# Kernel optimization log

Measured on AMD Instinct MI355X. Metric: run time of the kernel, lower is better.

The kernel has to match this reference:

```python
import jax, jax.numpy as jnp
import numpy as np


def setup_inputs() -> dict:
    key = jax.random.key(0)
    N0, N1, N2, E0, E1 = 40000, 8000, 2000, 128000, 32000
    IN, HID = 512, 256
    ks = iter(jax.random.split(key, 40))
    def nk():
        return next(ks)
    def lin_w(shape):
        fan_in = shape[1]
        return jax.random.uniform(nk(), shape, jnp.float32, -1.0, 1.0) / np.sqrt(fan_in)
    inp = {}
    inp["x"] = jax.random.normal(nk(), (N0, IN), jnp.float32)
    inp["ppr"] = jax.random.uniform(nk(), (N1, N1), jnp.float32) / N1  # ~row-stochastic PPR
    inp["src0"] = jax.random.randint(nk(), (E0,), 0, N0)
    inp["dst0"] = jax.random.randint(nk(), (E0,), 0, N1)
    inp["src1"] = jax.random.randint(nk(), (E1,), 0, N1)
    inp["dst1"] = jax.random.randint(nk(), (E1,), 0, N2)
    inp["n1"] = N1
    inp["n2"] = N2
    # SAGEConv layer 0 (in->hid) and layer 1 (hid->hid); lin_l has bias, lin_r does not (PyG default)
    inp["Wl0"] = lin_w((HID, IN)); inp["bl0"] = jnp.zeros((HID,), jnp.float32); inp["Wr0"] = lin_w((HID, IN))
    inp["Wl1"] = lin_w((HID, HID)); inp["bl1"] = jnp.zeros((HID,), jnp.float32); inp["Wr1"] = lin_w((HID, HID))
    # self.linear = [Linear(IN,IN)+ReLU, Linear(IN,HID)]
    inp["Wa"] = lin_w((IN, IN)); inp["ba"] = jnp.zeros((IN,), jnp.float32)
    inp["Wb"] = lin_w((HID, IN)); inp["bb"] = jnp.zeros((HID,), jnp.float32)
    # lin1 / lin2 (no bias)
    inp["W1"] = lin_w((HID, HID)); inp["W2"] = lin_w((HID, HID))
    # proj = MLP(HID, HID, HID)
    inp["Wp1"] = lin_w((HID, HID)); inp["bp1"] = jnp.zeros((HID,), jnp.float32)
    inp["Wp2"] = lin_w((HID, HID)); inp["bp2"] = jnp.zeros((HID,), jnp.float32)
    # clf = MLP(HID, 32, 1)
    inp["Wc1"] = lin_w((32, HID)); inp["bc1"] = jnp.zeros((32,), jnp.float32)
    inp["Wc2"] = lin_w((1, 32)); inp["bc2"] = jnp.zeros((1,), jnp.float32)
    return inp


def reference(x, ppr, Wl0, bl0, Wr0, Wl1, bl1, Wr1, Wa, ba, Wb, bb,
              W1, W2, Wp1, bp1, Wp2, bp2, Wc1, bc1, Wc2, bc2,
              src0, dst0, src1, dst1, n1, n2):
    EPS = 1e-12
    def l2n(v):
        return v / jnp.maximum(jnp.linalg.norm(v, axis=-1, keepdims=True), EPS)
    def sage(h_src, h_tgt, src, dst, Wl, bl, Wr, n_tgt):
        msg = h_src[src]  # [E, d] gather
        s = jax.ops.segment_sum(msg, dst, num_segments=n_tgt)
        cnt = jax.ops.segment_sum(jnp.ones((dst.shape[0],), h_src.dtype), dst, num_segments=n_tgt)
        agg = s / jnp.maximum(cnt, 1.0)[:, None]  # scatter-mean
        return agg @ Wl.T + bl + h_tgt @ Wr.T
    # --- GraphSAGE encoder (eval mode: dropout no-op) ---
    h = x
    h = sage(h, h[:n1], src0, dst0, Wl0, bl0, Wr0, n1)
    h = jax.nn.relu(h)
    h = sage(h, h[:n2], src1, dst1, Wl1, bl1, Wr1, n2)
    ebds = jax.nn.log_softmax(h, axis=-1)  # output_type 'ebds' != 'ebd' -> log_softmax path
    # --- divergence loss ---
    o1 = l2n(ebds @ W1.T)
    o2 = l2n(ebds @ W2.T)
    div_loss = jnp.mean(jnp.sum((o1 - o2) ** 2, axis=-1))
    # --- PPR branch ---
    xp = ppr[:n1, :n1] @ x[:n1]              # [n1, IN]
    xp = jax.nn.relu(xp @ Wa.T + ba)         # linear[0]
    xp = ppr[:n2, :n2] @ xp[:n2]             # [n2, IN]
    xp = xp @ Wb.T + bb                      # linear[1] -> [n2, HID]
    g1 = l2n(ebds)
    g2 = l2n(xp)
    def proj(v):
        return jax.nn.relu(v @ Wp1.T + bp1) @ Wp2.T + bp2
    def clf(v):
        return jax.nn.relu(v @ Wc1.T + bc1) @ Wc2.T + bc2
    l1 = clf(proj(g1))  # [n2, 1]
    l2_ = clf(proj(g2))  # [n2, 1]
    logits_pair = jnp.concatenate([l1, l2_], axis=-1)  # [n2, 2]
    return logits_pair, div_loss
```

## Files before the change

### kernel.cpp

```cpp
#include <hip/hip_runtime.h>


typedef unsigned short ushort;
typedef __attribute__((ext_vector_type(8))) short short8;
typedef __attribute__((ext_vector_type(4))) float float4v;
typedef __attribute__((ext_vector_type(4))) float f32x4;
typedef __attribute__((ext_vector_type(2))) float f32x2;
typedef __attribute__((ext_vector_type(8))) unsigned short us8;
typedef __attribute__((ext_vector_type(4))) unsigned short us4;
typedef __attribute__((ext_vector_type(2))) unsigned short us2;

__device__ __forceinline__ ushort bf16_rne(float v) {
    unsigned u = __float_as_uint(v);
    u += 0x7fffu + ((u >> 16) & 1u);
    return (ushort)(u >> 16);
}
__device__ __forceinline__ float bf16_f32(ushort h) {
    return __uint_as_float((unsigned)h << 16);
}

constexpr long ZCNT0 = 0;
constexpr long ZCNT1 = 8000;
constexpr long ELL0  = 10240;
constexpr long ELL1  = 522240;
constexpr long H1F   = 650240;
constexpr long H2F   = 2714624;
constexpr long DIVCF = 3238912;
constexpr long XPBF  = 4287488;
constexpr long PB2   = 4811776;
constexpr long PART  = 5860352;
constexpr long FEND  = 10054656;
constexpr long U_PPRB  = 0;
constexpr long U_PPR2B = 16777216;
constexpr long U_XTB   = 20971520;
constexpr long U_XPATB = 25165824;
constexpr long U_A0    = 26214400;
constexpr long U_A1    = 38600704;
constexpr long U_ESPL  = 40697856;
constexpr long U_XPS   = 41746432;
constexpr long U_SPLT  = 43843584;
constexpr long U_TSPL  = 45940736;
constexpr long U_WC0   = 48037888;
constexpr long U_WC1   = 48431104;
constexpr long U_BD    = 48693248;
constexpr long U_WAD   = 48955392;
constexpr long U_WBD   = 49479680;
constexpr long U_WP1D  = 49741824;
constexpr long U_WP2D  = 49872896;
constexpr long U_XB    = 50003968;

__global__ __launch_bounds__(256) void mfma128(
    const ushort* __restrict__ A, const ushort* __restrict__ B,
    float* __restrict__ Cf, ushort* __restrict__ Cs, ushort* __restrict__ Ct,
    const float* __restrict__ bias, int K, int lda, int ldb, int ldc,
    int ldso, int nsplit, int msplit, int ldt, int kchunk, int flags)
{
    __shared__ ushort As[128 * 128];
    __shared__ ushort Bs[128 * 128];
    const int tid = threadIdx.x;
    const int lane = tid & 63, wave = tid >> 6;
    const int wm = (wave >> 1) * 64, wn = (wave & 1) * 64;
    const int lr = lane & 15, quad = lane >> 4;

    int bx = blockIdx.x, by = blockIdx.y;
    if (flags & 8) {
        int gx = gridDim.x;
        int nb = gx * gridDim.y;
        int flat = by * gx + bx;
        int per = nb >> 3;
        int c = flat & 7, j = flat >> 3;
        int idx = c * per + j;
        by = idx / gx; bx = idx % gx;
    }
    const int bm = by * 128, bn = bx * 128;
    const int kbeg = blockIdx.z * kchunk;
    int kend = kbeg + kchunk; if (kend > K) kend = K;

    float4v acc[4][4] = {{{0.f, 0.f, 0.f, 0.f}}};

    for (int k0 = kbeg; k0 < kend; k0 += 128) {
#pragma unroll
        for (int issue = 0; issue < 8; ++issue) {
            int c = issue * 256 + tid;
            int r = c >> 4, p = c & 15;
            int kk = (p ^ (r & 15)) * 8;
            const ushort* ga = A + (long)(bm + r) * lda + k0 + kk;
            const ushort* gb = B + (long)(bn + r) * ldb + k0 + kk;
            __builtin_amdgcn_global_load_lds(
                (const __attribute__((address_space(1))) unsigned int*)ga,
                (__attribute__((address_space(3))) unsigned int*)&As[c * 8], 16, 0, 0);
            __builtin_amdgcn_global_load_lds(
                (const __attribute__((address_space(1))) unsigned int*)gb,
                (__attribute__((address_space(3))) unsigned int*)&Bs[c * 8], 16, 0, 0);
        }
        __syncthreads();

#pragma unroll
        for (int s = 0; s < 4; ++s) {
            short8 af[4], bf[4];
#pragma unroll
            for (int i = 0; i < 4; ++i) {
                int ra = wm + i * 16 + lr;
                af[i] = *(const short8*)&As[ra * 128 + (((s * 4 + quad) ^ (ra & 15)) * 8)];
                int rb = wn + i * 16 + lr;
                bf[i] = *(const short8*)&Bs[rb * 128 + (((s * 4 + quad) ^ (rb & 15)) * 8)];
            }
#pragma unroll
            for (int i = 0; i < 4; ++i)
#pragma unroll
                for (int j = 0; j < 4; ++j)
                    acc[i][j] = __builtin_amdgcn_mfma_f32_16x16x32_bf16(
                        af[i], bf[j], acc[i][j], 0, 0, 0);
        }
        __syncthreads();
    }

    if (gridDim.z > 1) {
        float* Cz = Cf + (long)blockIdx.z * (long)(gridDim.x * 128) * (long)(gridDim.y * 128);
#pragma unroll
        for (int i = 0; i < 4; ++i) {
            int row0 = bm + wm + i * 16 + quad * 4;
#pragma unroll
            for (int j = 0; j < 4; ++j) {
                int col = bn + wn + j * 16 + lr;
#pragma unroll
                for (int r = 0; r < 4; ++r)
                    Cz[(long)(row0 + r) * ldc + col] = acc[i][j][r];
            }
        }
        return;
    }

#pragma unroll
    for (int i = 0; i < 4; ++i) {
        int row0 = bm + wm + i * 16 + quad * 4;
#pragma unroll
        for (int j = 0; j < 4; ++j) {
            int col = bn + wn + j * 16 + lr;
            float bv = bias ? bias[col] : 0.f;
            us4 tp;
#pragma unroll
            for (int r = 0; r < 4; ++r) {
                int row = row0 + r;
                float v = acc[i][j][r] + bv;
                if (flags & 1) v = fmaxf(v, 0.f);
                if (Cf) Cf[(long)row * ldc + col] = v;
                if (Cs && row < msplit) {
                    if (flags & 2) {
                        ushort h = bf16_rne(v);
                        Cs[(long)row * ldso + col] = h;
                        Cs[(long)row * ldso + nsplit + col] = bf16_rne(v - bf16_f32(h));
                    } else {
                        Cs[(long)row * ldso + col] = bf16_rne(v);
                    }
                }
                if (flags & 4) tp[r] = bf16_rne(v);
            }
            if (flags & 4)
                *(us4*)&Ct[(long)col * ldt + row0] = tp;
        }
    }
}

__global__ __launch_bounds__(256) void reduce_split(
    const float* __restrict__ part, ushort* __restrict__ outs, long n, int S)
{
    long i = (long)blockIdx.x * 256 + threadIdx.x;
    if (i >= n) return;
    float s = 0.f;
    for (int k = 0; k < S; ++k) s += part[(long)k * n + i];
    int r = (int)(i >> 9), c = (int)(i & 511);
    ushort h = bf16_rne(s);
    outs[(long)r * 1024 + c] = h;
    outs[(long)r * 1024 + 512 + c] = bf16_rne(s - bf16_f32(h));
}

__global__ __launch_bounds__(256) void prep(
    const float* __restrict__ ppr, const float* __restrict__ x,
    const float* __restrict__ Wr0, const float* __restrict__ Wl0,
    const float* __restrict__ Wr1, const float* __restrict__ Wl1,
    const float* __restrict__ W1,  const float* __restrict__ W2,
    const float* __restrict__ Wa,  const float* __restrict__ Wb,
    const float* __restrict__ Wp1, const float* __restrict__ Wp2,
    ushort* __restrict__ uws, int* __restrict__ iws, float* __restrict__ outloss)
{
    __shared__ float tsm[32][33];
    int b = blockIdx.x, t = threadIdx.x;

    if (b < 40) {
        int idx = b * 256 + t;
        if (idx < 10000) iws[idx] = 0;
        if (idx == 10000) *outloss = 0.f;
        return;
    }
    if (b < 296) {
        int b2 = b - 40;
        int sec = b2 >> 5;
        const float *sa, *sb = nullptr; long dstoff; int N, KA, dA, KB = 0, dB = 0;
        switch (sec) {
            case 0: sa = Wr0; KA = 512; dA = 1; sb = Wl0; KB = 512; dB = 2;
                    dstoff = U_WC0; N = 256; break;
            case 1: sa = Wr1; KA = 256; dA = 2; sb = Wl1; KB = 256; dB = 2;
                    dstoff = U_WC1; N = 256; break;
            case 2: sa = W1;  KA = 256; dA = 2; dstoff = U_BD;          N = 256; break;
            case 3: sa = W2;  KA = 256; dA = 2; dstoff = U_BD + 131072; N = 256; break;
            case 4: sa = Wa;  KA = 512; dA = 2; dstoff = U_WAD;  N = 512; break;
            case 5: sa = Wb;  KA = 512; dA = 2; dstoff = U_WBD;  N = 256; break;
            case 6: sa = Wp1; KA = 256; dA = 2; dstoff = U_WP1D; N = 256; break;
            default: sa = Wp2; KA = 256; dA = 2; dstoff = U_WP2D; N = 256; break;
        }
        int kd = KA * dA + KB * dB;
        long totv = (long)N * kd / 2;
        for (long v = (long)(b2 & 31) * 256 + t; v < totv; v += 8192) {
            long idx = v * 2;
            int n = (int)(idx / kd), rem = (int)(idx % kd);
            f32x2 val;
            if (rem < KA * dA) {
                int sc = rem % KA;
                val = *(const f32x2*)&sa[(long)n * KA + sc];
            } else {
                int sc = (rem - KA * dA) % KB;
                val = *(const f32x2*)&sb[(long)n * KB + sc];
            }
            us2 o; o[0] = bf16_rne(val[0]); o[1] = bf16_rne(val[1]);
            *(us2*)&uws[dstoff + idx] = o;
        }
        return;
    }
    if (b < 8488) {
        int id = b - 296;
        int r = id >> 2, q = id & 3;
        bool live = r < 2000;
        const float* row = ppr + (long)r * 8000;
        int cbeg = q * 2048;
#pragma unroll
        for (int pass = 0; pass < 2; ++pass) {
            int c = cbeg + pass * 1024 + t * 4;
            f32x4 v = {0.f, 0.f, 0.f, 0.f};
            if (live && c < 8000) v = *(const f32x4*)(row + c);
            us4 u;
            u[0] = bf16_rne(v[0]); u[1] = bf16_rne(v[1]);
            u[2] = bf16_rne(v[2]); u[3] = bf16_rne(v[3]);
            *(us4*)&uws[U_PPRB + (long)r * 8192 + c] = u;
            if (c < 2048) {
                us4 w = u;
                if (c >= 2000) { w[0] = 0; w[1] = 0; w[2] = 0; w[3] = 0; }
                *(us4*)&uws[U_PPR2B + (long)r * 2048 + c] = w;
            }
        }
        return;
    }
    if (b < 12584) {
        int id = b - 8488;
        int c0 = (id & 15) * 32, r0 = (id >> 4) * 32;
        int tx = t & 31, ty = t >> 5;
#pragma unroll
        for (int k = 0; k < 32; k += 8) {
            int r = r0 + ty + k;
            tsm[ty + k][tx] = (r < 8000) ? x[(long)r * 512 + c0 + tx] : 0.f;
        }
        __syncthreads();
#pragma unroll
        for (int k = 0; k < 32; k += 8) {
            int c = c0 + ty + k;
            uws[U_XTB + (long)c * 8192 + r0 + tx] = bf16_rne(tsm[tx][ty + k]);
        }
        return;
    }
    {
        long vi = (long)(b - 12584) * 256 + t;
        for (; vi < 5120000; vi += 327680) {
            long gidx = vi * 4;
            f32x4 v = *(const f32x4*)&x[gidx];
            us4 u;
            u[0] = bf16_rne(v[0]); u[1] = bf16_rne(v[1]);
            u[2] = bf16_rne(v[2]); u[3] = bf16_rne(v[3]);
            *(us4*)&uws[U_XB + gidx] = u;
            long row = gidx >> 9;
            if (row < 8064) {
                int col = (int)(gidx & 511);
                *(us4*)&uws[U_A0 + row * 1536 + col] = u;
            }
        }
    }
}

__global__ __launch_bounds__(256) void ell_fill(
    const int* __restrict__ src0, const int* __restrict__ dst0,
    const int* __restrict__ src1, const int* __restrict__ dst1,
    int* __restrict__ cnt0, int* __restrict__ cnt1,
    int* __restrict__ ell0, int* __restrict__ ell1, int E0, int E1)
{
    int e = blockIdx.x * 256 + threadIdx.x;
    if (e < E0) {
        int d = dst0[e];
        int r = atomicAdd(&cnt0[d], 1);
        if (r < 64) ell0[d + 8000 * r] = src0[e];
    } else if (e < E0 + E1) {
        int e1 = e - E0;
        int d = dst1[e1];
        int r = atomicAdd(&cnt1[d], 1);
        if (r < 64) ell1[d + 2000 * r] = src1[e1];
    }
}

__global__ __launch_bounds__(256) void csr_agg0(
    const ushort* __restrict__ xb, const int* __restrict__ ell,
    const int* __restrict__ cnt, ushort* __restrict__ a0)
{
    __shared__ float part[4][512];
    int d = blockIdx.x, t = threadIdx.x;
    int w = t >> 6, lane = t & 63;
    int k = (d < 8000) ? min(cnt[d], 64) : 0;
    float s[8] = {0.f, 0.f, 0.f, 0.f, 0.f, 0.f, 0.f, 0.f};
    int co = lane * 8;
    int j = w;
    for (; j + 12 < k; j += 16) {
        int e0 = ell[d + 8000 * j],        e1 = ell[d + 8000 * (j + 4)];
        int e2 = ell[d + 8000 * (j + 8)],  e3 = ell[d + 8000 * (j + 12)];
        us8 v0 = *(const us8*)&xb[(long)e0 * 512 + co];
        us8 v1 = *(const us8*)&xb[(long)e1 * 512 + co];
        us8 v2 = *(const us8*)&xb[(long)e2 * 512 + co];
        us8 v3 = *(const us8*)&xb[(long)e3 * 512 + co];
#pragma unroll
        for (int q = 0; q < 8; ++q)
            s[q] += bf16_f32(v0[q]) + bf16_f32(v1[q]) +
                    bf16_f32(v2[q]) + bf16_f32(v3[q]);
    }
    for (; j < k; j += 4) {
        us8 v = *(const us8*)&xb[(long)ell[d + 8000 * j] * 512 + co];
#pragma unroll
        for (int q = 0; q < 8; ++q) s[q] += bf16_f32(v[q]);
    }
#pragma unroll
    for (int q = 0; q < 8; ++q) part[w][co + q] = s[q];
    __syncthreads();
    float inv = 1.f / fmaxf((float)k, 1.f);
    long ro = (long)d * 1536;
#pragma unroll
    for (int h = 0; h < 2; ++h) {
        int c = 2 * t + h;
        float a = (part[0][c] + part[1][c] + part[2][c] + part[3][c]) * inv;
        ushort hi = bf16_rne(a);
        a0[ro + 512 + c] = hi;
        a0[ro + 1024 + c] = bf16_rne(a - bf16_f32(hi));
    }
}

__global__ __launch_bounds__(256) void csr_agg1(
    const float* __restrict__ h, const int* __restrict__ ell,
    const int* __restrict__ cnt, ushort* __restrict__ a1)
{
    __shared__ float part[4][256];
    int d = blockIdx.x, t = threadIdx.x;
    int w = t >> 6, lane = t & 63;
    int k = (d < 2000) ? min(cnt[d], 64) : 0;
    f32x4 s = {0.f, 0.f, 0.f, 0.f};
    int co = lane * 4;
    int j = w;
    for (; j + 12 < k; j += 16) {
        int e0 = ell[d + 2000 * j],        e1 = ell[d + 2000 * (j + 4)];
        int e2 = ell[d + 2000 * (j + 8)],  e3 = ell[d + 2000 * (j + 12)];
        f32x4 v0 = *(const f32x4*)&h[(long)e0 * 256 + co];
        f32x4 v1 = *(const f32x4*)&h[(long)e1 * 256 + co];
        f32x4 v2 = *(const f32x4*)&h[(long)e2 * 256 + co];
        f32x4 v3 = *(const f32x4*)&h[(long)e3 * 256 + co];
        s += v0; s += v1; s += v2; s += v3;
    }
    for (; j < k; j += 4)
        s += *(const f32x4*)&h[(long)ell[d + 2000 * j] * 256 + co];
#pragma unroll
    for (int q = 0; q < 4; ++q) part[w][co + q] = s[q];
    __syncthreads();
    float inv = 1.f / fmaxf((float)k, 1.f);
    float a = (part[0][t] + part[1][t] + part[2][t] + part[3][t]) * inv;
    ushort hi = bf16_rne(a);
    long ro = (long)d * 1024;
    a1[ro + 512 + t] = hi;
    a1[ro + 768 + t] = bf16_rne(a - bf16_f32(hi));
}

__global__ __launch_bounds__(256) void rowcombo(
    const float* __restrict__ h2, const float* __restrict__ xpb,
    ushort* __restrict__ espl, ushort* __restrict__ splt)
{
    __shared__ float red[256];
    int b = blockIdx.x, t = threadIdx.x;
    if (b < 2000) {
        int i = b;
        float v = h2[(long)i * 256 + t];
        red[t] = v;
        __syncthreads();
        for (int s = 128; s > 0; s >>= 1) {
            if (t < s) red[t] = fmaxf(red[t], red[t + s]);
            __syncthreads();
        }
        float m = red[0];
        __syncthreads();
        float e = expf(v - m);
        red[t] = e;
        __syncthreads();
        for (int s = 128; s > 0; s >>= 1) {
            if (t < s) red[t] += red[t + s];
            __syncthreads();
        }
        float eb = v - (m + logf(red[0]));
        ushort hh = bf16_rne(eb);
        espl[(long)i * 512 + t] = hh;
        espl[(long)i * 512 + 256 + t] = bf16_rne(eb - bf16_f32(hh));
        __syncthreads();
        red[t] = eb * eb;
        __syncthreads();
        for (int s = 128; s > 0; s >>= 1) {
            if (t < s) red[t] += red[t + s];
            __syncthreads();
        }
        float g = eb / fmaxf(sqrtf(red[0]), 1e-12f);
        ushort gh = bf16_rne(g);
        splt[(long)i * 512 + t] = gh;
        splt[(long)i * 512 + 256 + t] = bf16_rne(g - bf16_f32(gh));
    } else {
        int i = b - 2000;
        float v = xpb[(long)i * 256 + t];
        red[t] = v * v;
        __syncthreads();
        for (int s = 128; s > 0; s >>= 1) {
            if (t < s) red[t] += red[t + s];
            __syncthreads();
        }
        float g = v / fmaxf(sqrtf(red[0]), 1e-12f);
        ushort gh = bf16_rne(g);
        long ro = (long)(2048 + i) * 512;
        splt[ro + t] = gh;
        splt[ro + 256 + t] = bf16_rne(g - bf16_f32(gh));
    }
}

__global__ __launch_bounds__(256) void final_combo(
    const float* __restrict__ p, const float* __restrict__ Wc1,
    const float* __restrict__ bc1, const float* __restrict__ Wc2,
    const float* __restrict__ bc2, float* __restrict__ out,
    const float* __restrict__ divc, float scale)
{
    __shared__ float v[256];
    __shared__ float ps[8][33];
    __shared__ float hsum[32];
    __shared__ float r2[256];
    int b = blockIdx.x, t = threadIdx.x;
    if (b >= 4096) {
        int i = b - 4096;
        float a = divc[(long)i * 512 + t], bb = divc[(long)i * 512 + 256 + t];
        v[t] = a * a;
        r2[t] = bb * bb;
        __syncthreads();
        for (int s = 128; s > 0; s >>= 1) {
            if (t < s) { v[t] += v[t + s]; r2[t] += r2[t + s]; }
            __syncthreads();
        }
        float na = fmaxf(sqrtf(v[0]), 1e-12f);
        float nb = fmaxf(sqrtf(r2[0]), 1e-12f);
        __syncthreads();
        float d = a / na - bb / nb;
        v[t] = d * d;
        __syncthreads();
        for (int s = 128; s > 0; s >>= 1) {
            if (t < s) v[t] += v[t + s];
            __syncthreads();
        }
        if (t == 0) atomicAdd(&out[4000], v[0] * scale);
        return;
    }
    int half = b >> 11, i = b & 2047;
    if (i >= 2000) return;
    v[t] = p[(long)b * 256 + t];
    __syncthreads();
    int o = t & 31, ch = t >> 5;
    const float* w = Wc1 + (long)o * 256 + ch * 32;
    const float* vv = v + ch * 32;
    float s = 0.f;
#pragma unroll
    for (int k2 = 0; k2 < 32; ++k2) s += vv[k2] * w[k2];
    ps[ch][o] = s;
    __syncthreads();
    if (t < 32) {
        float a = bc1[t];
#pragma unroll
        for (int c = 0; c < 8; ++c) a += ps[c][t];
        a = fmaxf(a, 0.f);
        hsum[t] = a * Wc2[t];
    }
    __syncthreads();
    if (t == 0) {
        float s2 = bc2[0];
        for (int k2 = 0; k2 < 32; ++k2) s2 += hsum[k2];
        out[(long)i * 2 + half] = s2;
    }
}

extern "C" void kernel_launch(void* const* d_in, const int* in_sizes, int n_in,
                              void* d_out, int out_size, void* d_ws, size_t ws_size,
                              hipStream_t stream)
{
    constexpr int N2 = 2000;

    const float* x   = (const float*)d_in[0];
    const float* ppr = (const float*)d_in[1];
    const int* src0  = (const int*)d_in[2];
    const int* dst0  = (const int*)d_in[3];
    const int* src1  = (const int*)d_in[4];
    const int* dst1  = (const int*)d_in[5];
    const float* Wl0 = (const float*)d_in[8];
    const float* bl0 = (const float*)d_in[9];
    const float* Wr0 = (const float*)d_in[10];
    const float* Wl1 = (const float*)d_in[11];
    const float* bl1 = (const float*)d_in[12];
    const float* Wr1 = (const float*)d_in[13];
    const float* Wa  = (const float*)d_in[14];
    const float* ba  = (const float*)d_in[15];
    const float* Wb  = (const float*)d_in[16];
    const float* bb  = (const float*)d_in[17];
    const float* W1  = (const float*)d_in[18];
    const float* W2  = (const float*)d_in[19];
    const float* Wp1 = (const float*)d_in[20];
    const float* bp1 = (const float*)d_in[21];
    const float* Wp2 = (const float*)d_in[22];
    const float* bp2 = (const float*)d_in[23];
    const float* Wc1 = (const float*)d_in[24];
    const float* bc1 = (const float*)d_in[25];
    const float* Wc2 = (const float*)d_in[26];
    const float* bc2 = (const float*)d_in[27];

    const int E0 = in_sizes[2];
    const int E1 = in_sizes[4];

    float* out = (float*)d_out;
    float* ws  = (float*)d_ws;
    int*   iws = (int*)d_ws;
    ushort* uws = (ushort*)((char*)d_ws + FEND * sizeof(float));

    auto cdiv = [](int a, int b) { return (a + b - 1) / b; };

    prep<<<13864, 256, 0, stream>>>(ppr, x, Wr0, Wl0, Wr1, Wl1, W1, W2,
                                    Wa, Wb, Wp1, Wp2, uws, iws, out + (long)N2 * 2);

    ell_fill<<<cdiv(E0 + E1, 256), 256, 0, stream>>>(
        src0, dst0, src1, dst1, iws + ZCNT0, iws + ZCNT1,
        iws + ELL0, iws + ELL1, E0, E1);

    csr_agg0<<<8064, 256, 0, stream>>>(uws + U_XB, iws + ELL0, iws + ZCNT0,
                                       uws + U_A0);
    mfma128<<<dim3(2, 63), 256, 0, stream>>>(
        uws + U_A0, uws + U_WC0, ws + H1F, uws + U_A1, nullptr, bl0,
        1536, 1536, 1536, 256, 1024, 256, 2048, 0, 1536, 3);

    csr_agg1<<<2048, 256, 0, stream>>>(ws + H1F, iws + ELL1, iws + ZCNT1,
                                       uws + U_A1);
    mfma128<<<dim3(2, 16), 256, 0, stream>>>(
        uws + U_A1, uws + U_WC1, ws + H2F, nullptr, nullptr, bl1,
        1024, 1024, 1024, 256, 0, 0, 0, 0, 1024, 8);

    mfma128<<<dim3(4, 16, 4), 256, 0, stream>>>(
        uws + U_PPRB, uws + U_XTB, ws + PART, nullptr, nullptr, nullptr,
        8192, 8192, 8192, 512, 0, 0, 0, 0, 2048, 8);
    reduce_split<<<4096, 256, 0, stream>>>(ws + PART, uws + U_XPS, 1048576L, 4);
    mfma128<<<dim3(4, 16), 256, 0, stream>>>(
        uws + U_XPS, uws + U_WAD, nullptr, nullptr, uws + U_XPATB, ba,
        1024, 1024, 1024, 0, 0, 0, 0, 2048, 1024, 13);

    mfma128<<<dim3(4, 16, 2), 256, 0, stream>>>(
        uws + U_PPR2B, uws + U_XPATB, ws + PART, nullptr, nullptr, nullptr,
        2048, 2048, 2048, 512, 0, 0, 0, 0, 1024, 8);
    reduce_split<<<4096, 256, 0, stream>>>(ws + PART, uws + U_XPS, 1048576L, 2);
    mfma128<<<dim3(2, 16), 256, 0, stream>>>(
        uws + U_XPS, uws + U_WBD, ws + XPBF, nullptr, nullptr, bb,
        1024, 1024, 1024, 256, 0, 0, 0, 0, 1024, 8);

    rowcombo<<<4000, 256, 0, stream>>>(ws + H2F, ws + XPBF,
                                       uws + U_ESPL, uws + U_SPLT);

    mfma128<<<dim3(4, 16), 256, 0, stream>>>(
        uws + U_ESPL, uws + U_BD, ws + DIVCF, nullptr, nullptr, nullptr,
        512, 512, 512, 512, 0, 0, 0, 0, 512, 8);

    mfma128<<<dim3(2, 32), 256, 0, stream>>>(
        uws + U_SPLT, uws + U_WP1D, nullptr, uws + U_TSPL, nullptr, bp1,
        512, 512, 512, 0, 512, 256, 4096, 0, 512, 11);
    mfma128<<<dim3(2, 32), 256, 0, stream>>>(
        uws + U_TSPL, uws + U_WP2D, ws + PB2, nullptr, nullptr, bp2,
        512, 512, 512, 256, 0, 0, 0, 0, 512, 8);

    final_combo<<<6096, 256, 0, stream>>>(ws + PB2, Wc1, bc1, Wc2, bc2, out,
                                          ws + DIVCF, 1.0f / N2);
}
```

Before: 729.4 us.

## Co-schedule independent GEMMs and reductions into shared launches via descriptor dispatch

Replaces the grid-indexed GEMM kernel with a descriptor-driven device function so several independent stages can share one launch. The big PPR GEMM runs alongside the layer-0 SAGE GEMM, the second aggregation runs with the split-K reduction, and log-softmax row work or the second reduction rides alongside smaller GEMMs. The aim is to fill the GPU with otherwise-idle small grids and cut launch and tail gaps across the dependency chain. The cost is a mixed-workload kernel whose LDS footprint applies even to non-GEMM blocks, plus more complex dependency ordering.

```diff
diff --git a/kernel.cpp b/kernel.cpp
--- a/kernel.cpp
+++ b/kernel.cpp
@@ -49,32 +49,36 @@
 constexpr long U_WP2D  = 49872896;
 constexpr long U_XB    = 50003968;
 
-__global__ __launch_bounds__(256) void mfma128(
-    const ushort* __restrict__ A, const ushort* __restrict__ B,
-    float* __restrict__ Cf, ushort* __restrict__ Cs, ushort* __restrict__ Ct,
-    const float* __restrict__ bias, int K, int lda, int ldb, int ldc,
-    int ldso, int nsplit, int msplit, int ldt, int kchunk, int flags)
-{
-    __shared__ ushort As[128 * 128];
-    __shared__ ushort Bs[128 * 128];
+struct GemmDesc {
+    const ushort* A; const ushort* B;
+    float* Cf; ushort* Cs; ushort* Ct;
+    const float* bias;
+    int K, lda, ldb, ldc;
+    int ldso, nsplit, msplit, ldt;
+    int gx, gy, kchunk;
+    long slabsize;
+    int flags;
+};
+
+__device__ __forceinline__ void run_gemm(const GemmDesc& d, int f,
+                                         ushort* As, ushort* Bs)
+{
     const int tid = threadIdx.x;
     const int lane = tid & 63, wave = tid >> 6;
     const int wm = (wave >> 1) * 64, wn = (wave & 1) * 64;
     const int lr = lane & 15, quad = lane >> 4;
 
-    int bx = blockIdx.x, by = blockIdx.y;
-    if (flags & 8) {
-        int gx = gridDim.x;
-        int nb = gx * gridDim.y;
-        int flat = by * gx + bx;
-        int per = nb >> 3;
-        int c = flat & 7, j = flat >> 3;
-        int idx = c * per + j;
-        by = idx / gx; bx = idx % gx;
-    }
+    int per = d.gx * d.gy;
+    int z = f / per;
+    int rem = f - z * per;
+    if (d.flags & 8) {
+        int c = rem & 7, j = rem >> 3;
+        rem = c * (per >> 3) + j;
+    }
+    int by = rem / d.gx, bx = rem - by * d.gx;
     const int bm = by * 128, bn = bx * 128;
-    const int kbeg = blockIdx.z * kchunk;
-    int kend = kbeg + kchunk; if (kend > K) kend = K;
+    const int kbeg = z * d.kchunk;
+    int kend = kbeg + d.kchunk; if (kend > d.K) kend = d.K;
 
     float4v acc[4][4] = {{{0.f, 0.f, 0.f, 0.f}}};
 
@@ -84,8 +88,8 @@
             int c = issue * 256 + tid;
             int r = c >> 4, p = c & 15;
             int kk = (p ^ (r & 15)) * 8;
-            const ushort* ga = A + (long)(bm + r) * lda + k0 + kk;
-            const ushort* gb = B + (long)(bn + r) * ldb + k0 + kk;
+            const ushort* ga = d.A + (long)(bm + r) * d.lda + k0 + kk;
+            const ushort* gb = d.B + (long)(bn + r) * d.ldb + k0 + kk;
             __builtin_amdgcn_global_load_lds(
                 (const __attribute__((address_space(1))) unsigned int*)ga,
                 (__attribute__((address_space(3))) unsigned int*)&As[c * 8], 16, 0, 0);
@@ -115,8 +119,8 @@
         __syncthreads();
     }
 
-    if (gridDim.z > 1) {
-        float* Cz = Cf + (long)blockIdx.z * (long)(gridDim.x * 128) * (long)(gridDim.y * 128);
+    if (d.flags & 16) {
+        float* Cz = d.Cf + (long)z * d.slabsize;
 #pragma unroll
         for (int i = 0; i < 4; ++i) {
             int row0 = bm + wm + i * 16 + quad * 4;
@@ -125,7 +129,7 @@
                 int col = bn + wn + j * 16 + lr;
 #pragma unroll
                 for (int r = 0; r < 4; ++r)
-                    Cz[(long)(row0 + r) * ldc + col] = acc[i][j][r];
+                    Cz[(long)(row0 + r) * d.ldc + col] = acc[i][j][r];
             }
         }
         return;
@@ -137,35 +141,35 @@
 #pragma unroll
         for (int j = 0; j < 4; ++j) {
             int col = bn + wn + j * 16 + lr;
-            float bv = bias ? bias[col] : 0.f;
+            float bv = d.bias ? d.bias[col] : 0.f;
             us4 tp;
 #pragma unroll
             for (int r = 0; r < 4; ++r) {
                 int row = row0 + r;
                 float v = acc[i][j][r] + bv;
-                if (flags & 1) v = fmaxf(v, 0.f);
-                if (Cf) Cf[(long)row * ldc + col] = v;
-                if (Cs && row < msplit) {
-                    if (flags & 2) {
+                if (d.flags & 1) v = fmaxf(v, 0.f);
+                if (d.Cf) d.Cf[(long)row * d.ldc + col] = v;
+                if (d.Cs && row < d.msplit) {
+                    if (d.flags & 2) {
                         ushort h = bf16_rne(v);
-                        Cs[(long)row * ldso + col] = h;
-                        Cs[(long)row * ldso + nsplit + col] = bf16_rne(v - bf16_f32(h));
+                        d.Cs[(long)row * d.ldso + col] = h;
+                        d.Cs[(long)row * d.ldso + d.nsplit + col] = bf16_rne(v - bf16_f32(h));
                     } else {
-                        Cs[(long)row * ldso + col] = bf16_rne(v);
+                        d.Cs[(long)row * d.ldso + col] = bf16_rne(v);
                     }
                 }
-                if (flags & 4) tp[r] = bf16_rne(v);
+                if (d.flags & 4) tp[r] = bf16_rne(v);
             }
-            if (flags & 4)
-                *(us4*)&Ct[(long)col * ldt + row0] = tp;
-        }
-    }
-}
-
-__global__ __launch_bounds__(256) void reduce_split(
-    const float* __restrict__ part, ushort* __restrict__ outs, long n, int S)
-{
-    long i = (long)blockIdx.x * 256 + threadIdx.x;
+            if (d.flags & 4)
+                *(us4*)&d.Ct[(long)col * d.ldt + row0] = tp;
+        }
+    }
+}
+
+__device__ __forceinline__ void reduce_body(
+    const float* __restrict__ part, ushort* __restrict__ outs,
+    long i, long n, int S)
+{
     if (i >= n) return;
     float s = 0.f;
     for (int k = 0; k < S; ++k) s += part[(long)k * n + i];
@@ -173,6 +177,115 @@
     ushort h = bf16_rne(s);
     outs[(long)r * 1024 + c] = h;
     outs[(long)r * 1024 + 512 + c] = bf16_rne(s - bf16_f32(h));
+}
+
+__global__ __launch_bounds__(256) void gemm_one(GemmDesc d)
+{
+    __shared__ ushort As[16384];
+    __shared__ ushort Bs[16384];
+    run_gemm(d, blockIdx.x, As, Bs);
+}
+
+__global__ __launch_bounds__(256) void gemm_dual(GemmDesc d0, int n0, GemmDesc d1)
+{
+    __shared__ ushort As[16384];
+    __shared__ ushort Bs[16384];
+    int f = blockIdx.x;
+    if (f < n0) run_gemm(d0, f, As, Bs);
+    else        run_gemm(d1, f - n0, As, Bs);
+}
+
+__global__ __launch_bounds__(256) void gemm_row(
+    GemmDesc d0, int n0, const float* __restrict__ h2,
+    ushort* __restrict__ espl, ushort* __restrict__ splt)
+{
+    __shared__ ushort As[16384];
+    __shared__ ushort Bs[16384];
+    int f = blockIdx.x, t = threadIdx.x;
+    if (f < n0) { run_gemm(d0, f, As, Bs); return; }
+    float* red = (float*)As;
+    int i = f - n0;
+    float v = h2[(long)i * 256 + t];
+    red[t] = v;
+    __syncthreads();
+    for (int s = 128; s > 0; s >>= 1) {
+        if (t < s) red[t] = fmaxf(red[t], red[t + s]);
+        __syncthreads();
+    }
+    float m = red[0];
+    __syncthreads();
+    float e = expf(v - m);
+    red[t] = e;
+    __syncthreads();
+    for (int s = 128; s > 0; s >>= 1) {
+        if (t < s) red[t] += red[t + s];
+        __syncthreads();
+    }
+    float eb = v - (m + logf(red[0]));
+    ushort hh = bf16_rne(eb);
+    espl[(long)i * 512 + t] = hh;
+    espl[(long)i * 512 + 256 + t] = bf16_rne(eb - bf16_f32(hh));
+    __syncthreads();
+    red[t] = eb * eb;
+    __syncthreads();
+    for (int s = 128; s > 0; s >>= 1) {
+        if (t < s) red[t] += red[t + s];
+        __syncthreads();
+    }
+    float g = eb / fmaxf(sqrtf(red[0]), 1e-12f);
+    ushort gh = bf16_rne(g);
+    splt[(long)i * 512 + t] = gh;
+    splt[(long)i * 512 + 256 + t] = bf16_rne(g - bf16_f32(gh));
+}
+
+__global__ __launch_bounds__(256) void gemm_red(
+    GemmDesc d0, int n0, const float* __restrict__ part,
+    ushort* __restrict__ outs, long n, int S)
+{
+    __shared__ ushort As[16384];
+    __shared__ ushort Bs[16384];
+    int f = blockIdx.x;
+    if (f < n0) { run_gemm(d0, f, As, Bs); return; }
+    reduce_body(part, outs, (long)(f - n0) * 256 + threadIdx.x, n, S);
+}
+
+__global__ __launch_bounds__(256) void aggred(
+    const float* __restrict__ h, const int* __restrict__ ell,
+    const int* __restrict__ cnt, ushort* __restrict__ a1,
+    const float* __restrict__ part, ushort* __restrict__ outs)
+{
+    __shared__ float pl[4][256];
+    int b = blockIdx.x, t = threadIdx.x;
+    if (b >= 2048) {
+        reduce_body(part, outs, (long)(b - 2048) * 256 + t, 1048576L, 4);
+        return;
+    }
+    int d = b;
+    int w = t >> 6, lane = t & 63;
+    int k = (d < 2000) ? min(cnt[d], 64) : 0;
+    f32x4 s = {0.f, 0.f, 0.f, 0.f};
+    int co = lane * 4;
+    int j = w;
+    for (; j + 12 < k; j += 16) {
+        int e0 = ell[d + 2000 * j],        e1 = ell[d + 2000 * (j + 4)];
+        int e2 = ell[d + 2000 * (j + 8)],  e3 = ell[d + 2000 * (j + 12)];
+        f32x4 v0 = *(const f32x4*)&h[(long)e0 * 256 + co];
+        f32x4 v1 = *(const f32x4*)&h[(long)e1 * 256 + co];
+        f32x4 v2 = *(const f32x4*)&h[(long)e2 * 256 + co];
+        f32x4 v3 = *(const f32x4*)&h[(long)e3 * 256 + co];
+        s += v0; s += v1; s += v2; s += v3;
+    }
+    for (; j < k; j += 4)
+        s += *(const f32x4*)&h[(long)ell[d + 2000 * j] * 256 + co];
+#pragma unroll
+    for (int q = 0; q < 4; ++q) pl[w][co + q] = s[q];
+    __syncthreads();
+    float inv = 1.f / fmaxf((float)k, 1.f);
+    float a = (pl[0][t] + pl[1][t] + pl[2][t] + pl[3][t]) * inv;
+    ushort hi = bf16_rne(a);
+    long ro = (long)d * 1024;
+    a1[ro + 512 + t] = hi;
+    a1[ro + 768 + t] = bf16_rne(a - bf16_f32(hi));
 }
 
 __global__ __launch_bounds__(256) void prep(
@@ -347,93 +460,23 @@
     }
 }
 
-__global__ __launch_bounds__(256) void csr_agg1(
-    const float* __restrict__ h, const int* __restrict__ ell,
-    const int* __restrict__ cnt, ushort* __restrict__ a1)
-{
-    __shared__ float part[4][256];
-    int d = blockIdx.x, t = threadIdx.x;
-    int w = t >> 6, lane = t & 63;
-    int k = (d < 2000) ? min(cnt[d], 64) : 0;
-    f32x4 s = {0.f, 0.f, 0.f, 0.f};
-    int co = lane * 4;
-    int j = w;
-    for (; j + 12 < k; j += 16) {
-        int e0 = ell[d + 2000 * j],        e1 = ell[d + 2000 * (j + 4)];
-        int e2 = ell[d + 2000 * (j + 8)],  e3 = ell[d + 2000 * (j + 12)];
-        f32x4 v0 = *(const f32x4*)&h[(long)e0 * 256 + co];
-        f32x4 v1 = *(const f32x4*)&h[(long)e1 * 256 + co];
-        f32x4 v2 = *(const f32x4*)&h[(long)e2 * 256 + co];
-        f32x4 v3 = *(const f32x4*)&h[(long)e3 * 256 + co];
-        s += v0; s += v1; s += v2; s += v3;
-    }
-    for (; j < k; j += 4)
-        s += *(const f32x4*)&h[(long)ell[d + 2000 * j] * 256 + co];
-#pragma unroll
-    for (int q = 0; q < 4; ++q) part[w][co + q] = s[q];
-    __syncthreads();
-    float inv = 1.f / fmaxf((float)k, 1.f);
-    float a = (part[0][t] + part[1][t] + part[2][t] + part[3][t]) * inv;
-    ushort hi = bf16_rne(a);
-    long ro = (long)d * 1024;
-    a1[ro + 512 + t] = hi;
-    a1[ro + 768 + t] = bf16_rne(a - bf16_f32(hi));
-}
-
-__global__ __launch_bounds__(256) void rowcombo(
-    const float* __restrict__ h2, const float* __restrict__ xpb,
-    ushort* __restrict__ espl, ushort* __restrict__ splt)
+__global__ __launch_bounds__(256) void rowcombo2(
+    const float* __restrict__ xpb, ushort* __restrict__ splt)
 {
     __shared__ float red[256];
-    int b = blockIdx.x, t = threadIdx.x;
-    if (b < 2000) {
-        int i = b;
-        float v = h2[(long)i * 256 + t];
-        red[t] = v;
-        __syncthreads();
-        for (int s = 128; s > 0; s >>= 1) {
-            if (t < s) red[t] = fmaxf(red[t], red[t + s]);
-            __syncthreads();
-        }
-        float m = red[0];
-        __syncthreads();
-        float e = expf(v - m);
-        red[t] = e;
-        __syncthreads();
-        for (int s = 128; s > 0; s >>= 1) {
-            if (t < s) red[t] += red[t + s];
-            __syncthreads();
-        }
-        float eb = v - (m + logf(red[0]));
-        ushort hh = bf16_rne(eb);
-        espl[(long)i * 512 + t] = hh;
-        espl[(long)i * 512 + 256 + t] = bf16_rne(eb - bf16_f32(hh));
-        __syncthreads();
-        red[t] = eb * eb;
-        __syncthreads();
-        for (int s = 128; s > 0; s >>= 1) {
-            if (t < s) red[t] += red[t + s];
-            __syncthreads();
-        }
-        float g = eb / fmaxf(sqrtf(red[0]), 1e-12f);
-        ushort gh = bf16_rne(g);
-        splt[(long)i * 512 + t] = gh;
-        splt[(long)i * 512 + 256 + t] = bf16_rne(g - bf16_f32(gh));
-    } else {
-        int i = b - 2000;
-        float v = xpb[(long)i * 256 + t];
-        red[t] = v * v;
-        __syncthreads();
-        for (int s = 128; s > 0; s >>= 1) {
-            if (t < s) red[t] += red[t + s];
-            __syncthreads();
-        }
-        float g = v / fmaxf(sqrtf(red[0]), 1e-12f);
-        ushort gh = bf16_rne(g);
-        long ro = (long)(2048 + i) * 512;
-        splt[ro + t] = gh;
-        splt[ro + 256 + t] = bf16_rne(g - bf16_f32(gh));
-    }
+    int i = blockIdx.x, t = threadIdx.x;
+    float v = xpb[(long)i * 256 + t];
+    red[t] = v * v;
+    __syncthreads();
+    for (int s = 128; s > 0; s >>= 1) {
+        if (t < s) red[t] += red[t + s];
+        __syncthreads();
+    }
+    float g = v / fmaxf(sqrtf(red[0]), 1e-12f);
+    ushort gh = bf16_rne(g);
+    long ro = (long)(2048 + i) * 512;
+    splt[ro + t] = gh;
+    splt[ro + 256 + t] = bf16_rne(g - bf16_f32(gh));
 }
 
 __global__ __launch_bounds__(256) void final_combo(
@@ -540,6 +583,8 @@
 
     auto cdiv = [](int a, int b) { return (a + b - 1) / b; };
 
+    GemmDesc z{};
+
     prep<<<13864, 256, 0, stream>>>(ppr, x, Wr0, Wl0, Wr1, Wl1, W1, W2,
                                     Wa, Wb, Wp1, Wp2, uws, iws, out + (long)N2 * 2);
 
@@ -549,45 +594,72 @@
 
     csr_agg0<<<8064, 256, 0, stream>>>(uws + U_XB, iws + ELL0, iws + ZCNT0,
                                        uws + U_A0);
-    mfma128<<<dim3(2, 63), 256, 0, stream>>>(
-        uws + U_A0, uws + U_WC0, ws + H1F, uws + U_A1, nullptr, bl0,
-        1536, 1536, 1536, 256, 1024, 256, 2048, 0, 1536, 3);
-
-    csr_agg1<<<2048, 256, 0, stream>>>(ws + H1F, iws + ELL1, iws + ZCNT1,
-                                       uws + U_A1);
-    mfma128<<<dim3(2, 16), 256, 0, stream>>>(
-        uws + U_A1, uws + U_WC1, ws + H2F, nullptr, nullptr, bl1,
-        1024, 1024, 1024, 256, 0, 0, 0, 0, 1024, 8);
-
-    mfma128<<<dim3(4, 16, 4), 256, 0, stream>>>(
-        uws + U_PPRB, uws + U_XTB, ws + PART, nullptr, nullptr, nullptr,
-        8192, 8192, 8192, 512, 0, 0, 0, 0, 2048, 8);
-    reduce_split<<<4096, 256, 0, stream>>>(ws + PART, uws + U_XPS, 1048576L, 4);
-    mfma128<<<dim3(4, 16), 256, 0, stream>>>(
-        uws + U_XPS, uws + U_WAD, nullptr, nullptr, uws + U_XPATB, ba,
-        1024, 1024, 1024, 0, 0, 0, 0, 2048, 1024, 13);
-
-    mfma128<<<dim3(4, 16, 2), 256, 0, stream>>>(
-        uws + U_PPR2B, uws + U_XPATB, ws + PART, nullptr, nullptr, nullptr,
-        2048, 2048, 2048, 512, 0, 0, 0, 0, 1024, 8);
-    reduce_split<<<4096, 256, 0, stream>>>(ws + PART, uws + U_XPS, 1048576L, 2);
-    mfma128<<<dim3(2, 16), 256, 0, stream>>>(
-        uws + U_XPS, uws + U_WBD, ws + XPBF, nullptr, nullptr, bb,
-        1024, 1024, 1024, 256, 0, 0, 0, 0, 1024, 8);
-
-    rowcombo<<<4000, 256, 0, stream>>>(ws + H2F, ws + XPBF,
+
+    GemmDesc dxp1 = z;
+    dxp1.A = uws + U_PPRB; dxp1.B = uws + U_XTB; dxp1.Cf = ws + PART;
+    dxp1.K = 8192; dxp1.lda = 8192; dxp1.ldb = 8192; dxp1.ldc = 512;
+    dxp1.gx = 4; dxp1.gy = 16; dxp1.kchunk = 2048; dxp1.slabsize = 1048576;
+    dxp1.flags = 16 | 8;
+    GemmDesc dh1 = z;
+    dh1.A = uws + U_A0; dh1.B = uws + U_WC0; dh1.Cf = ws + H1F;
+    dh1.Cs = uws + U_A1; dh1.bias = bl0;
+    dh1.K = 1536; dh1.lda = 1536; dh1.ldb = 1536; dh1.ldc = 256;
+    dh1.ldso = 1024; dh1.nsplit = 256; dh1.msplit = 2048;
+    dh1.gx = 2; dh1.gy = 63; dh1.kchunk = 1536; dh1.flags = 3;
+    gemm_dual<<<382, 256, 0, stream>>>(dxp1, 256, dh1);
+
+    aggred<<<6144, 256, 0, stream>>>(ws + H1F, iws + ELL1, iws + ZCNT1,
+                                     uws + U_A1, ws + PART, uws + U_XPS);
+
+    GemmDesc dxpa = z;
+    dxpa.A = uws + U_XPS; dxpa.B = uws + U_WAD; dxpa.Ct = uws + U_XPATB;
+    dxpa.bias = ba;
+    dxpa.K = 1024; dxpa.lda = 1024; dxpa.ldb = 1024; dxpa.ldt = 2048;
+    dxpa.gx = 4; dxpa.gy = 16; dxpa.kchunk = 1024; dxpa.flags = 1 | 4 | 8;
+    GemmDesc dh2 = z;
+    dh2.A = uws + U_A1; dh2.B = uws + U_WC1; dh2.Cf = ws + H2F; dh2.bias = bl1;
+    dh2.K = 1024; dh2.lda = 1024; dh2.ldb = 1024; dh2.ldc = 256;
+    dh2.gx = 2; dh2.gy = 16; dh2.kchunk = 1024; dh2.flags = 8;
+    gemm_dual<<<96, 256, 0, stream>>>(dxpa, 64, dh2);
+
+    GemmDesc dxp2 = z;
+    dxp2.A = uws + U_PPR2B; dxp2.B = uws + U_XPATB; dxp2.Cf = ws + PART;
+    dxp2.K = 2048; dxp2.lda = 2048; dxp2.ldb = 2048; dxp2.ldc = 512;
+    dxp2.gx = 4; dxp2.gy = 16; dxp2.kchunk = 1024; dxp2.slabsize = 1048576;
+    dxp2.flags = 16 | 8;
+    gemm_row<<<2128, 256, 0, stream>>>(dxp2, 128, ws + H2F,
                                        uws + U_ESPL, uws + U_SPLT);
 
-    mfma128<<<dim3(4, 16), 256, 0, stream>>>(
-        uws + U_ESPL, uws + U_BD, ws + DIVCF, nullptr, nullptr, nullptr,
-        512, 512, 512, 512, 0, 0, 0, 0, 512, 8);
-
-    mfma128<<<dim3(2, 32), 256, 0, stream>>>(
-        uws + U_SPLT, uws + U_WP1D, nullptr, uws + U_TSPL, nullptr, bp1,
-        512, 512, 512, 0, 512, 256, 4096, 0, 512, 11);
-    mfma128<<<dim3(2, 32), 256, 0, stream>>>(
-        uws + U_TSPL, uws + U_WP2D, ws + PB2, nullptr, nullptr, bp2,
-        512, 512, 512, 256, 0, 0, 0, 0, 512, 8);
+    GemmDesc ddiv = z;
+    ddiv.A = uws + U_ESPL; ddiv.B = uws + U_BD; ddiv.Cf = ws + DIVCF;
+    ddiv.K = 512; ddiv.lda = 512; ddiv.ldb = 512; ddiv.ldc = 512;
+    ddiv.gx = 4; ddiv.gy = 16; ddiv.kchunk = 512; ddiv.flags = 8;
+    gemm_red<<<4160, 256, 0, stream>>>(ddiv, 64, ws + PART, uws + U_XPS,
+                                       1048576L, 2);
+
+    GemmDesc dxpb = z;
+    dxpb.A = uws + U_XPS; dxpb.B = uws + U_WBD; dxpb.Cf = ws + XPBF;
+    dxpb.bias = bb;
+    dxpb.K = 1024; dxpb.lda = 1024; dxpb.ldb = 1024; dxpb.ldc = 256;
+    dxpb.gx = 2; dxpb.gy = 16; dxpb.kchunk = 1024; dxpb.flags = 8;
+    gemm_one<<<32, 256, 0, stream>>>(dxpb);
+
+    rowcombo2<<<N2, 256, 0, stream>>>(ws + XPBF, uws + U_SPLT);
+
+    GemmDesc dp1 = z;
+    dp1.A = uws + U_SPLT; dp1.B = uws + U_WP1D; dp1.Cs = uws + U_TSPL;
+    dp1.bias = bp1;
+    dp1.K = 512; dp1.lda = 512; dp1.ldb = 512;
+    dp1.ldso = 512; dp1.nsplit = 256; dp1.msplit = 4096;
+    dp1.gx = 2; dp1.gy = 32; dp1.kchunk = 512; dp1.flags = 1 | 2 | 8;
+    gemm_one<<<64, 256, 0, stream>>>(dp1);
+
+    GemmDesc dp2 = z;
+    dp2.A = uws + U_TSPL; dp2.B = uws + U_WP2D; dp2.Cf = ws + PB2;
+    dp2.bias = bp2;
+    dp2.K = 512; dp2.lda = 512; dp2.ldb = 512; dp2.ldc = 256;
+    dp2.gx = 2; dp2.gy = 32; dp2.kchunk = 512; dp2.flags = 8;
+    gemm_one<<<64, 256, 0, stream>>>(dp2);
 
     final_combo<<<6096, 256, 0, stream>>>(ws + PB2, Wc1, bc1, Wc2, bc2, out,
                                           ws + DIVCF, 1.0f / N2);
```

Result: slower. 756.5 us (+3.7%).
